# Kernel optimization log

Hardware: AMD Instinct MI355X
Metric: run time of the kernel (lower is better)

Reference implementation:

```python
import jax, jax.numpy as jnp
import numpy as np

NUM_HEADS = 32
HEAD_DIM = 128
HIDDEN = NUM_HEADS * HEAD_DIM  # 4096
ROPE_BASE = 10000.0
VISION_TOKEN_TYPE = 1


def vision_expert_mask(token_type_ids):
    # vision_token_mask[:, :-1] = (tt[:, :-1]==1) & (tt[:, 1:]==1); last col False
    tt = token_type_ids
    m = (tt[:, :-1] == VISION_TOKEN_TYPE) & (tt[:, 1:] == VISION_TOKEN_TYPE)
    return jnp.concatenate([m, jnp.zeros((tt.shape[0], 1), dtype=bool)], axis=1)


def rotary_cos_sin(position_ids, head_dim, dtype):
    inv_freq = 1.0 / (ROPE_BASE ** (jnp.arange(0, head_dim, 2, dtype=jnp.float32) / head_dim))
    freqs = position_ids.astype(jnp.float32)[..., None] * inv_freq  # [B,S,Dh/2]
    emb = jnp.concatenate([freqs, freqs], axis=-1)  # [B,S,Dh]
    return jnp.cos(emb).astype(dtype), jnp.sin(emb).astype(dtype)


def rotate_half(x):
    d = x.shape[-1] // 2
    return jnp.concatenate([-x[..., d:], x[..., :d]], axis=-1)


def setup_inputs() -> dict:
    key = jax.random.key(0)
    ks = jax.random.split(key, 5)
    B, S = 2, 2048
    hidden_states = jax.random.normal(ks[0], (B, S, HIDDEN), dtype=jnp.float32)
    token_type_ids = jax.random.randint(ks[1], (B, S), 0, 2, dtype=jnp.int64)
    position_ids = jnp.broadcast_to(jnp.arange(S, dtype=jnp.int64)[None, :], (B, S))
    scale = 0.02
    w_vis_qkv = jax.random.normal(ks[2], (HIDDEN, 3 * HIDDEN), dtype=jnp.float32) * scale
    w_lang_qkv = jax.random.normal(ks[3], (HIDDEN, 3 * HIDDEN), dtype=jnp.float32) * scale
    w_vis_dense = jax.random.normal(ks[4], (HIDDEN, HIDDEN), dtype=jnp.float32) * scale
    w_lang_dense = jax.random.normal(jax.random.fold_in(key, 7), (HIDDEN, HIDDEN), dtype=jnp.float32) * scale
    return dict(hidden_states=hidden_states, token_type_ids=token_type_ids,
                position_ids=position_ids, w_vis_qkv=w_vis_qkv, w_lang_qkv=w_lang_qkv,
                w_vis_dense=w_vis_dense, w_lang_dense=w_lang_dense)


def reference(hidden_states, token_type_ids, position_ids,
              w_vis_qkv, w_lang_qkv, w_vis_dense, w_lang_dense):
    B, S, D = hidden_states.shape
    vm = vision_expert_mask(token_type_ids)  # [B,S] bool

    # 2-expert QKV dispatch (mask-select between the two expert GEMMs)
    qkv = jnp.where(vm[..., None],
                    hidden_states @ w_vis_qkv,
                    hidden_states @ w_lang_qkv)  # [B,S,3D]
    q, k, v = jnp.split(qkv, 3, axis=-1)
    q = q.reshape(B, S, NUM_HEADS, HEAD_DIM)
    k = k.reshape(B, S, NUM_HEADS, HEAD_DIM)
    v = v.reshape(B, S, NUM_HEADS, HEAD_DIM)

    # rotary embedding on q, k
    cos, sin = rotary_cos_sin(position_ids, HEAD_DIM, q.dtype)  # [B,S,Dh]
    cos, sin = cos[:, :, None, :], sin[:, :, None, :]
    q = q * cos + rotate_half(q) * sin
    k = k * cos + rotate_half(k) * sin

    # causal attention (dense equivalent of the paged-attention call)
    scores = jnp.einsum('bqhd,bkhd->bhqk', q, k) / jnp.sqrt(jnp.array(HEAD_DIM, q.dtype))
    causal = jnp.tril(jnp.ones((S, S), dtype=bool))
    scores = jnp.where(causal[None, None], scores, jnp.finfo(scores.dtype).min)
    probs = jax.nn.softmax(scores, axis=-1)
    ctx = jnp.einsum('bhqk,bkhd->bqhd', probs, v).reshape(B, S, D)

    # 2-expert output dense dispatch
    attn_output = jnp.where(vm[..., None],
                            ctx @ w_vis_dense,
                            ctx @ w_lang_dense)
    return attn_output
```

## Files before the change

### kernel.cpp

```cpp
#include <hip/hip_runtime.h>
#include <math.h>

#define SEQ     2048
#define NB      2
#define NHEADS  32
#define DHEAD   128
#define HID     4096
#define NQKV    12288
#define T_TOKENS (NB*SEQ)

typedef _Float16 half8 __attribute__((ext_vector_type(8)));
typedef float v4f __attribute__((ext_vector_type(4)));

__device__ __forceinline__ void gload_lds16(const void* g, void* l) {
    __builtin_amdgcn_global_load_lds(
        (__attribute__((address_space(1))) void*)(void*)(g),
        (__attribute__((address_space(3))) void*)(unsigned)(unsigned long long)(l),
        16, 0, 0);
}

__device__ __forceinline__ v4f mfma16(half8 a, half8 b, v4f c) {
    return __builtin_amdgcn_mfma_f32_16x16x32_f16(a, b, c, 0, 0, 0);
}

__global__ void route_kernel(const int* __restrict__ tt, int* counts, int* idx) {
    int t = blockIdx.x * blockDim.x + threadIdx.x;
    if (t >= T_TOKENS) return;
    int s = t & (SEQ - 1);
    bool vm = (s < SEQ - 1) && (tt[t] == 1) && (tt[t + 1] == 1);
    int e = vm ? 0 : 1;
    int p = atomicAdd(&counts[e], 1);
    idx[e * T_TOKENS + p] = t;
}

__global__ void rope_table_kernel(const int* __restrict__ pos_ids, float2* __restrict__ tab) {
    int i = blockIdx.x * blockDim.x + threadIdx.x;
    if (i >= T_TOKENS * 64) return;
    int tok = i >> 6, j = i & 63;
    float invf = (float)pow(10000.0, -(double)j * (1.0 / 64.0));
    float ang = (float)pos_ids[tok] * invf;
    double ds, dc;
    sincos((double)ang, &ds, &dc);
    tab[i] = make_float2((float)dc, (float)ds);
}

__global__ void cvt_f32_f16(const float* __restrict__ src, _Float16* __restrict__ dst, int n4) {
    int i = blockIdx.x * blockDim.x + threadIdx.x;
    if (i >= n4) return;
    float4 v = ((const float4*)src)[i];
    union { _Float16 h[4]; uint2 u; } p;
    p.h[0] = (_Float16)v.x; p.h[1] = (_Float16)v.y;
    p.h[2] = (_Float16)v.z; p.h[3] = (_Float16)v.w;
    ((uint2*)dst)[i] = p.u;
}

__global__ void transpose_cvt(const float* __restrict__ W, _Float16* __restrict__ WT,
                              int K, int N) {
    __shared__ _Float16 t[64][72];
    const int n0 = blockIdx.x * 64, k0 = blockIdx.y * 64;
    const int cr = threadIdx.x & 15, rr = threadIdx.x >> 4;
#pragma unroll
    for (int it = 0; it < 4; ++it) {
        int r = rr + it * 16;
        float4 v = *(const float4*)&W[(size_t)(k0 + r) * N + n0 + cr * 4];
        t[cr*4+0][r] = (_Float16)v.x; t[cr*4+1][r] = (_Float16)v.y;
        t[cr*4+2][r] = (_Float16)v.z; t[cr*4+3][r] = (_Float16)v.w;
    }
    __syncthreads();
#pragma unroll
    for (int it = 0; it < 4; ++it) {
        int r = rr + it * 16;
        union { _Float16 h[4]; uint2 u; } p;
#pragma unroll
        for (int j = 0; j < 4; ++j) p.h[j] = t[r][cr*4+j];
        *(uint2*)&WT[(size_t)(n0 + r) * K + k0 + cr * 4] = p.u;
    }
}

__global__ void transpose_v(const _Float16* __restrict__ vin, _Float16* __restrict__ vout) {
    __shared__ _Float16 t[64][72];
    const int s0 = blockIdx.x * 64;
    const int d0 = blockIdx.y * 64;
    const int bh = blockIdx.z;
    const int b = bh >> 5, h = bh & 31;
    const int cr = threadIdx.x & 15, rr = threadIdx.x >> 4;
#pragma unroll
    for (int it = 0; it < 4; ++it) {
        int sl = rr + it * 16;
        union { _Float16 h4[4]; uint2 u; } p;
        p.u = *(const uint2*)&vin[(size_t)(b * SEQ + s0 + sl) * HID + h * DHEAD + d0 + cr * 4];
#pragma unroll
        for (int j = 0; j < 4; ++j) t[cr*4+j][sl] = p.h4[j];
    }
    __syncthreads();
#pragma unroll
    for (int it = 0; it < 4; ++it) {
        int dl = rr + it * 16;
        union { _Float16 h4[4]; uint2 u; } p;
#pragma unroll
        for (int j = 0; j < 4; ++j) p.h4[j] = t[dl][cr*4+j];
        *(uint2*)&vout[((size_t)bh * DHEAD + d0 + dl) * SEQ + s0 + cr * 4] = p.u;
    }
}

template <int MODE, int NCT>
__global__ __launch_bounds__(256, 3)
void gemm_expert(const _Float16* __restrict__ A,
                 const _Float16* __restrict__ BT0,
                 const _Float16* __restrict__ BT1,
                 const int* __restrict__ counts,
                 const int* __restrict__ idx_all,
                 const float2* __restrict__ rope,
                 _Float16* __restrict__ qbuf,
                 _Float16* __restrict__ kbuf,
                 _Float16* __restrict__ vbuf,
                 float* __restrict__ out) {
    const int e = blockIdx.z;
    const int count = counts[e];

    const int f   = blockIdx.x + NCT * blockIdx.y;
    const int xcd = f & 7;
    const int g   = f >> 3;
    const int c   = g >> 6;
    const int wi  = g & 63;
    const int rt  = wi >> 1;
    const int ct  = xcd * (NCT / 8) + c * 2 + (wi & 1);

    if (rt * 128 >= count) return;
    const int* idx = idx_all + e * T_TOKENS;
    const _Float16* BT = e ? BT1 : BT0;

    __shared__ _Float16 sA[3][128 * 32];
    __shared__ _Float16 sB[3][128 * 32];

    const int tid = threadIdx.x;
    const int w = tid >> 6, lane = tid & 63;
    const int col = lane & 15, quad = lane >> 4;
    const int wm = w >> 1, wn = w & 1;

    const int r0 = (w * 2 + 0) * 16 + (lane >> 2);
    const int r1 = (w * 2 + 1) * 16 + (lane >> 2);
    int g0 = rt * 128 + r0; if (g0 > count - 1) g0 = count - 1;
    int g1 = rt * 128 + r1; if (g1 > count - 1) g1 = count - 1;
    const int tok0 = idx[g0], tok1 = idx[g1];
    const int schk = (lane & 3) ^ ((lane >> 3) & 3);
    const _Float16* ag0 = A + (size_t)tok0 * HID + schk * 8;
    const _Float16* ag1 = A + (size_t)tok1 * HID + schk * 8;
    const _Float16* bg0 = BT + (size_t)(ct * 128 + r0) * HID + schk * 8;
    const _Float16* bg1 = BT + (size_t)(ct * 128 + r1) * HID + schk * 8;
    const int sa_off0 = (w * 2 + 0) * 512;
    const int sa_off1 = (w * 2 + 1) * 512;

    v4f acc[4][4];
#pragma unroll
    for (int i = 0; i < 4; ++i)
#pragma unroll
        for (int j = 0; j < 4; ++j) { v4f z = {0.f, 0.f, 0.f, 0.f}; acc[i][j] = z; }

    const int kofq = (quad ^ ((col >> 1) & 3)) * 8;

    auto stage = [&](int buf) {
        gload_lds16(ag0, &sA[buf][sa_off0]); gload_lds16(ag1, &sA[buf][sa_off1]);
        gload_lds16(bg0, &sB[buf][sa_off0]); gload_lds16(bg1, &sB[buf][sa_off1]);
        ag0 += 32; ag1 += 32; bg0 += 32; bg1 += 32;
    };
    auto compute = [&](int cur) {
        half8 a[4], b[4];
#pragma unroll
        for (int i = 0; i < 4; ++i)
            a[i] = *(const half8*)&sA[cur][(wm * 64 + i * 16 + col) * 32 + kofq];
#pragma unroll
        for (int j = 0; j < 4; ++j)
            b[j] = *(const half8*)&sB[cur][((wn + 2 * j) * 16 + col) * 32 + kofq];
#pragma unroll
        for (int i = 0; i < 4; ++i)
#pragma unroll
            for (int j = 0; j < 4; ++j)
                acc[i][j] = mfma16(a[i], b[j], acc[i][j]);
    };

    const int NK = HID / 32;
    stage(0); stage(1);

    int cur = 0, nxt = 2;
    for (int kt = 0; kt < NK - 2; ++kt) {
        asm volatile("s_waitcnt vmcnt(4)" ::: "memory");
        __builtin_amdgcn_s_barrier();
        asm volatile("" ::: "memory");
        stage(nxt);
        compute(cur);
        cur = (cur == 2) ? 0 : cur + 1;
        nxt = (nxt == 2) ? 0 : nxt + 1;
    }
    asm volatile("s_waitcnt vmcnt(4)" ::: "memory");
    __builtin_amdgcn_s_barrier();
    asm volatile("" ::: "memory");
    compute(cur);
    cur = (cur == 2) ? 0 : cur + 1;
    asm volatile("s_waitcnt vmcnt(0)" ::: "memory");
    __builtin_amdgcn_s_barrier();
    asm volatile("" ::: "memory");
    compute(cur);

    const int n0 = ct * 128;
    if (MODE == 1) {
#pragma unroll
        for (int i = 0; i < 4; ++i)
#pragma unroll
            for (int r = 0; r < 4; ++r) {
                int rg = rt * 128 + wm * 64 + i * 16 + quad * 4 + r;
                if (rg >= count) continue;
                int tok = idx[rg];
                float* dst = out + (size_t)tok * HID + n0;
#pragma unroll
                for (int j = 0; j < 4; ++j) dst[(wn + 2 * j) * 16 + col] = acc[i][j][r];
            }
    } else {
        const int sec = n0 >> 12;
        const int h = (n0 >> 7) & 31;
#pragma unroll
        for (int i = 0; i < 4; ++i)
#pragma unroll
            for (int r = 0; r < 4; ++r) {
                int rg = rt * 128 + wm * 64 + i * 16 + quad * 4 + r;
                if (rg >= count) continue;
                int tok = idx[rg];
                int b = tok >> 11, s = tok & (SEQ - 1);
                if (sec == 2) {
                    _Float16* dst = vbuf + (size_t)tok * HID + h * DHEAD;
#pragma unroll
                    for (int j = 0; j < 4; ++j) dst[(wn + 2 * j) * 16 + col] = (_Float16)acc[i][j][r];
                } else {
                    _Float16* dst = (sec ? kbuf : qbuf) + ((size_t)(b * NHEADS + h) * SEQ + s) * DHEAD;
                    const float2* tp = rope + (size_t)tok * 64;
#pragma unroll
                    for (int j = 0; j < 2; ++j) {
                        int d = (wn + 2 * j) * 16 + col;
                        float2 cs = tp[d];
                        float x = acc[i][j][r], y = acc[i][j + 2][r];
                        dst[d]      = (_Float16)(x * cs.x - y * cs.y);
                        dst[d + 64] = (_Float16)(y * cs.x + x * cs.y);
                    }
                }
            }
    }
}

__global__ __launch_bounds__(256, 2)
void attn_kernel(const _Float16* __restrict__ qbuf,
                 const _Float16* __restrict__ kbuf,
                 const _Float16* __restrict__ vt,
                 _Float16* __restrict__ ctx) {
    const int f   = blockIdx.x;
    const int xcd = f & 7;
    const int t   = f >> 3;
    const int s   = t & 31;
    const int rr  = t >> 5;
    const int u   = s & 15, g = s >> 4;
    const int bh  = xcd * 8 + rr * 2 + g;
    const int qt  = (rr & 1) ? (15 - u) : u;

    const int b = bh >> 5, h = bh & 31;
    const int tid = threadIdx.x;
    const int w = tid >> 6, lane = tid & 63;
    const int col = lane & 15, quad = lane >> 4;

    __shared__ _Float16 sK[2][64 * 128];
    __shared__ _Float16 sV[2][128 * 64];
    __shared__ _Float16 sP[128 * 64];

    half8 qf[2][4];
    const _Float16 qscale = (_Float16)0.08838834764831845f;
#pragma unroll
    for (int mt = 0; mt < 2; ++mt)
#pragma unroll
        for (int kc = 0; kc < 4; ++kc) {
            int row = qt * 128 + w * 32 + mt * 16 + col;
            half8 v = *(const half8*)&qbuf[((size_t)bh * SEQ + row) * DHEAD + kc * 32 + quad * 8];
            qf[mt][kc] = v * qscale;
        }

    float mrow[2][4], lrow[2][4];
    v4f o[2][8];
#pragma unroll
    for (int mt = 0; mt < 2; ++mt)
#pragma unroll
        for (int r = 0; r < 4; ++r) { mrow[mt][r] = -3.0e38f; lrow[mt][r] = 0.f; }
#pragma unroll
    for (int i = 0; i < 2; ++i)
#pragma unroll
        for (int j = 0; j < 8; ++j) { v4f z = {0.f, 0.f, 0.f, 0.f}; o[i][j] = z; }

    const int cxor = col & 7;
    const int vs_chk = (lane & 7) ^ (lane >> 3);
    const int nkt = 2 * qt + 2;

    const _Float16* kg0 = kbuf + (size_t)bh * SEQ * DHEAD;
    const _Float16* vg0 = vt + (size_t)bh * DHEAD * SEQ;

    auto stage = [&](int kt, int buf) {
        const _Float16* kg = kg0 + (size_t)kt * 64 * DHEAD;
        const _Float16* vg = vg0 + kt * 64;
#pragma unroll
        for (int op = 0; op < 4; ++op) {
            int r0 = (w * 4 + op) * 4;
            int krow = r0 + quad;
            int kcs = col ^ (krow & 7);
            gload_lds16(kg + (size_t)krow * DHEAD + kcs * 8, &sK[buf][r0 * 128]);
            int d0 = (w * 4 + op) * 8;
            int vrow = d0 + (lane >> 3);
            gload_lds16(vg + (size_t)vrow * SEQ + vs_chk * 8, &sV[buf][d0 * 64]);
        }
    };

    stage(0, 0);
    __syncthreads();

    for (int kt = 0; kt < nkt; ++kt) {
        const int cur = kt & 1;
        if (kt + 1 < nkt) stage(kt + 1, cur ^ 1);

        v4f sc[2][4];
#pragma unroll
        for (int i = 0; i < 2; ++i)
#pragma unroll
            for (int j = 0; j < 4; ++j) { v4f z = {0.f, 0.f, 0.f, 0.f}; sc[i][j] = z; }
#pragma unroll
        for (int kc = 0; kc < 4; ++kc) {
            const int kof = ((kc * 4 + quad) ^ cxor) * 8;
#pragma unroll
            for (int nt = 0; nt < 4; ++nt) {
                half8 bf = *(const half8*)&sK[cur][(size_t)(nt * 16 + col) * 128 + kof];
                sc[0][nt] = mfma16(qf[0][kc], bf, sc[0][nt]);
                sc[1][nt] = mfma16(qf[1][kc], bf, sc[1][nt]);
            }
        }

        if (kt >= 2 * qt) {
#pragma unroll
            for (int mt = 0; mt < 2; ++mt)
#pragma unroll
                for (int nt = 0; nt < 4; ++nt)
#pragma unroll
                    for (int r = 0; r < 4; ++r) {
                        int rowa = qt * 128 + w * 32 + mt * 16 + quad * 4 + r;
                        int cola = kt * 64 + nt * 16 + col;
                        if (cola > rowa) sc[mt][nt][r] = -3.0e38f;
                    }
        }

#pragma unroll
        for (int mt = 0; mt < 2; ++mt)
#pragma unroll
            for (int r = 0; r < 4; ++r) {
                float mx = sc[mt][0][r];
#pragma unroll
                for (int nt = 1; nt < 4; ++nt) mx = fmaxf(mx, sc[mt][nt][r]);
                mx = fmaxf(mx, __shfl_xor(mx, 1));
                mx = fmaxf(mx, __shfl_xor(mx, 2));
                mx = fmaxf(mx, __shfl_xor(mx, 4));
                mx = fmaxf(mx, __shfl_xor(mx, 8));
                float newm = fmaxf(mrow[mt][r], mx);
                float alpha = __expf(mrow[mt][r] - newm);
                mrow[mt][r] = newm;
                float rs = 0.f;
#pragma unroll
                for (int nt = 0; nt < 4; ++nt) {
                    float p = __expf(sc[mt][nt][r] - newm);
                    sc[mt][nt][r] = p;
                    rs += p;
                }
                rs += __shfl_xor(rs, 1); rs += __shfl_xor(rs, 2);
                rs += __shfl_xor(rs, 4); rs += __shfl_xor(rs, 8);
                lrow[mt][r] = lrow[mt][r] * alpha + rs;
#pragma unroll
                for (int nt = 0; nt < 8; ++nt) o[mt][nt][r] *= alpha;
            }

#pragma unroll
        for (int mt = 0; mt < 2; ++mt)
#pragma unroll
            for (int nt = 0; nt < 4; ++nt)
#pragma unroll
                for (int r = 0; r < 4; ++r) {
                    int rp = w * 32 + mt * 16 + quad * 4 + r;
                    int colh = nt * 16 + col;
                    int c = (colh >> 3) ^ (rp & 7);
                    sP[(size_t)rp * 64 + c * 8 + (colh & 7)] = (_Float16)sc[mt][nt][r];
                }

#pragma unroll
        for (int kc = 0; kc < 2; ++kc) {
            const int kof = ((kc * 4 + quad) ^ cxor) * 8;
            half8 p0 = *(const half8*)&sP[(size_t)(w * 32 + col) * 64 + kof];
            half8 p1 = *(const half8*)&sP[(size_t)(w * 32 + 16 + col) * 64 + kof];
#pragma unroll
            for (int nt = 0; nt < 8; ++nt) {
                half8 vf = *(const half8*)&sV[cur][(size_t)(nt * 16 + col) * 64 + kof];
                o[0][nt] = mfma16(p0, vf, o[0][nt]);
                o[1][nt] = mfma16(p1, vf, o[1][nt]);
            }
        }

        __syncthreads();
    }

#pragma unroll
    for (int mt = 0; mt < 2; ++mt)
#pragma unroll
        for (int r = 0; r < 4; ++r) {
            int rowa = qt * 128 + w * 32 + mt * 16 + quad * 4 + r;
            float inv = 1.0f / lrow[mt][r];
            _Float16* dst = ctx + ((size_t)b * SEQ + rowa) * HID + h * DHEAD;
#pragma unroll
            for (int nt = 0; nt < 8; ++nt)
                dst[nt * 16 + col] = (_Float16)(o[mt][nt][r] * inv);
        }
}

extern "C" void kernel_launch(void* const* d_in, const int* in_sizes, int n_in,
                              void* d_out, int out_size, void* d_ws, size_t ws_size,
                              hipStream_t stream) {
    const float* hidden = (const float*)d_in[0];
    const int*   tt     = (const int*)d_in[1];
    const int*   pos    = (const int*)d_in[2];
    const float* wvq    = (const float*)d_in[3];
    const float* wlq    = (const float*)d_in[4];
    const float* wvd    = (const float*)d_in[5];
    const float* wld    = (const float*)d_in[6];
    float* out = (float*)d_out;

    char* ws = (char*)d_ws;
    size_t off = 0;
    auto alloc = [&](size_t bytes) {
        char* p = ws + off;
        off += (bytes + 255) & ~(size_t)255;
        return p;
    };
    const size_t TOKB = (size_t)T_TOKENS * HID * sizeof(_Float16);
    _Float16* h16  = (_Float16*)alloc(TOKB);
    _Float16* wvqT = (_Float16*)alloc((size_t)NQKV * HID * 2);
    _Float16* wlqT = (_Float16*)alloc((size_t)NQKV * HID * 2);
    _Float16* wvdT = (_Float16*)alloc((size_t)HID * HID * 2);
    _Float16* wldT = (_Float16*)alloc((size_t)HID * HID * 2);
    _Float16* qb   = (_Float16*)alloc(TOKB);
    _Float16* kb   = (_Float16*)alloc(TOKB);
    _Float16* vtmp = (_Float16*)alloc(TOKB);
    int* counts = (int*)alloc(2 * sizeof(int));
    int* idx    = (int*)alloc(2 * T_TOKENS * sizeof(int));
    float2* rope = (float2*)alloc((size_t)T_TOKENS * 64 * sizeof(float2));
    _Float16* vT  = h16;
    _Float16* ctx = vtmp;

    hipMemsetAsync(counts, 0, 2 * sizeof(int), stream);
    route_kernel<<<T_TOKENS / 256, 256, 0, stream>>>(tt, counts, idx);
    rope_table_kernel<<<(T_TOKENS * 64) / 256, 256, 0, stream>>>(pos, rope);
    cvt_f32_f16<<<(T_TOKENS * HID / 4) / 256, 256, 0, stream>>>(hidden, h16, T_TOKENS * HID / 4);
    transpose_cvt<<<dim3(NQKV / 64, HID / 64), 256, 0, stream>>>(wvq, wvqT, HID, NQKV);
    transpose_cvt<<<dim3(NQKV / 64, HID / 64), 256, 0, stream>>>(wlq, wlqT, HID, NQKV);
    transpose_cvt<<<dim3(HID / 64, HID / 64), 256, 0, stream>>>(wvd, wvdT, HID, HID);
    transpose_cvt<<<dim3(HID / 64, HID / 64), 256, 0, stream>>>(wld, wldT, HID, HID);
    gemm_expert<0, NQKV / 128><<<dim3(NQKV / 128, T_TOKENS / 128, 2), 256, 0, stream>>>(
        h16, wvqT, wlqT, counts, idx, rope, qb, kb, vtmp, nullptr);
    transpose_v<<<dim3(SEQ / 64, DHEAD / 64, NB * NHEADS), 256, 0, stream>>>(vtmp, vT);
    attn_kernel<<<dim3(16 * NB * NHEADS), 256, 0, stream>>>(qb, kb, vT, ctx);
    gemm_expert<1, HID / 128><<<dim3(HID / 128, T_TOKENS / 128, 2), 256, 0, stream>>>(
        ctx, wvdT, wldT, counts, idx, nullptr, nullptr, nullptr, nullptr, out);
}
```

Before: 1.549 ms.

## Pair causal q-tiles per attention block and raise priority around MFMA

Each attention block now processes two complementary query tiles (u and 15-u) of the same head, sharing each staged K/V tile between them, which balances causal work per block and halves K/V loads. The grid is halved accordingly. s_setprio is raised around the MFMA loops in both the GEMM and attention kernels to favor matrix issue over other waves. Doubling the accumulators and Q fragments raises register pressure and may cause spills or lower occupancy.

Result: slower. 1.913 ms (+23.5%).

```diff
diff --git a/kernel.cpp b/kernel.cpp
--- a/kernel.cpp
+++ b/kernel.cpp
@@ -172,11 +172,13 @@
 #pragma unroll
         for (int j = 0; j < 4; ++j)
             b[j] = *(const half8*)&sB[cur][((wn + 2 * j) * 16 + col) * 32 + kofq];
+        __builtin_amdgcn_s_setprio(1);
 #pragma unroll
         for (int i = 0; i < 4; ++i)
 #pragma unroll
             for (int j = 0; j < 4; ++j)
                 acc[i][j] = mfma16(a[i], b[j], acc[i][j]);
+        __builtin_amdgcn_s_setprio(0);
     };
 
     const int NK = HID / 32;
@@ -254,11 +256,9 @@
     const int f   = blockIdx.x;
     const int xcd = f & 7;
     const int t   = f >> 3;
-    const int s   = t & 31;
-    const int rr  = t >> 5;
-    const int u   = s & 15, g = s >> 4;
-    const int bh  = xcd * 8 + rr * 2 + g;
-    const int qt  = (rr & 1) ? (15 - u) : u;
+    const int u   = t & 7;
+    const int bh  = xcd * 8 + (t >> 3);
+    const int qtA = u, qtB = 15 - u;
 
     const int b = bh >> 5, h = bh & 31;
     const int tid = threadIdx.x;
@@ -269,31 +269,39 @@
     __shared__ _Float16 sV[2][128 * 64];
     __shared__ _Float16 sP[128 * 64];
 
-    half8 qf[2][4];
     const _Float16 qscale = (_Float16)0.08838834764831845f;
+    half8 qfA[2][4], qfB[2][4];
 #pragma unroll
     for (int mt = 0; mt < 2; ++mt)
 #pragma unroll
         for (int kc = 0; kc < 4; ++kc) {
-            int row = qt * 128 + w * 32 + mt * 16 + col;
-            half8 v = *(const half8*)&qbuf[((size_t)bh * SEQ + row) * DHEAD + kc * 32 + quad * 8];
-            qf[mt][kc] = v * qscale;
-        }
-
-    float mrow[2][4], lrow[2][4];
-    v4f o[2][8];
+            int rowA = qtA * 128 + w * 32 + mt * 16 + col;
+            qfA[mt][kc] = *(const half8*)&qbuf[((size_t)bh * SEQ + rowA) * DHEAD + kc * 32 + quad * 8] * qscale;
+            int rowB = qtB * 128 + w * 32 + mt * 16 + col;
+            qfB[mt][kc] = *(const half8*)&qbuf[((size_t)bh * SEQ + rowB) * DHEAD + kc * 32 + quad * 8] * qscale;
+        }
+
+    float mA[2][4], lA[2][4], mB[2][4], lB[2][4];
+    v4f oA[2][8], oB[2][8];
 #pragma unroll
     for (int mt = 0; mt < 2; ++mt)
 #pragma unroll
-        for (int r = 0; r < 4; ++r) { mrow[mt][r] = -3.0e38f; lrow[mt][r] = 0.f; }
+        for (int r = 0; r < 4; ++r) {
+            mA[mt][r] = -3.0e38f; lA[mt][r] = 0.f;
+            mB[mt][r] = -3.0e38f; lB[mt][r] = 0.f;
+        }
 #pragma unroll
     for (int i = 0; i < 2; ++i)
 #pragma unroll
-        for (int j = 0; j < 8; ++j) { v4f z = {0.f, 0.f, 0.f, 0.f}; o[i][j] = z; }
+        for (int j = 0; j < 8; ++j) {
+            v4f z = {0.f, 0.f, 0.f, 0.f};
+            oA[i][j] = z; oB[i][j] = z;
+        }
 
     const int cxor = col & 7;
     const int vs_chk = (lane & 7) ^ (lane >> 3);
-    const int nkt = 2 * qt + 2;
+    const int nkt  = 2 * qtB + 2;
+    const int nktA = 2 * qtA + 2;
 
     const _Float16* kg0 = kbuf + (size_t)bh * SEQ * DHEAD;
     const _Float16* vg0 = vt + (size_t)bh * DHEAD * SEQ;
@@ -313,18 +321,14 @@
         }
     };
 
-    stage(0, 0);
-    __syncthreads();
-
-    for (int kt = 0; kt < nkt; ++kt) {
-        const int cur = kt & 1;
-        if (kt + 1 < nkt) stage(kt + 1, cur ^ 1);
-
+    auto proc = [&](const half8 (&qf)[2][4], float (&mrow)[2][4], float (&lrow)[2][4],
+                    v4f (&o)[2][8], int qt, int kt, int cur) {
         v4f sc[2][4];
 #pragma unroll
         for (int i = 0; i < 2; ++i)
 #pragma unroll
             for (int j = 0; j < 4; ++j) { v4f z = {0.f, 0.f, 0.f, 0.f}; sc[i][j] = z; }
+        __builtin_amdgcn_s_setprio(1);
 #pragma unroll
         for (int kc = 0; kc < 4; ++kc) {
             const int kof = ((kc * 4 + quad) ^ cxor) * 8;
@@ -335,6 +339,7 @@
                 sc[1][nt] = mfma16(qf[1][kc], bf, sc[1][nt]);
             }
         }
+        __builtin_amdgcn_s_setprio(0);
 
         if (kt >= 2 * qt) {
 #pragma unroll
@@ -389,6 +394,7 @@
                     sP[(size_t)rp * 64 + c * 8 + (colh & 7)] = (_Float16)sc[mt][nt][r];
                 }
 
+        __builtin_amdgcn_s_setprio(1);
 #pragma unroll
         for (int kc = 0; kc < 2; ++kc) {
             const int kof = ((kc * 4 + quad) ^ cxor) * 8;
@@ -401,21 +407,35 @@
                 o[1][nt] = mfma16(p1, vf, o[1][nt]);
             }
         }
-
+        __builtin_amdgcn_s_setprio(0);
+    };
+
+    stage(0, 0);
+    __syncthreads();
+
+    for (int kt = 0; kt < nkt; ++kt) {
+        const int cur = kt & 1;
+        if (kt + 1 < nkt) stage(kt + 1, cur ^ 1);
+        proc(qfB, mB, lB, oB, qtB, kt, cur);
+        if (kt < nktA) proc(qfA, mA, lA, oA, qtA, kt, cur);
         __syncthreads();
     }
 
-#pragma unroll
-    for (int mt = 0; mt < 2; ++mt)
-#pragma unroll
-        for (int r = 0; r < 4; ++r) {
-            int rowa = qt * 128 + w * 32 + mt * 16 + quad * 4 + r;
-            float inv = 1.0f / lrow[mt][r];
-            _Float16* dst = ctx + ((size_t)b * SEQ + rowa) * HID + h * DHEAD;
-#pragma unroll
-            for (int nt = 0; nt < 8; ++nt)
-                dst[nt * 16 + col] = (_Float16)(o[mt][nt][r] * inv);
-        }
+    auto writeo = [&](float (&lrow)[2][4], v4f (&o)[2][8], int qt) {
+#pragma unroll
+        for (int mt = 0; mt < 2; ++mt)
+#pragma unroll
+            for (int r = 0; r < 4; ++r) {
+                int rowa = qt * 128 + w * 32 + mt * 16 + quad * 4 + r;
+                float inv = 1.0f / lrow[mt][r];
+                _Float16* dst = ctx + ((size_t)b * SEQ + rowa) * HID + h * DHEAD;
+#pragma unroll
+                for (int nt = 0; nt < 8; ++nt)
+                    dst[nt * 16 + col] = (_Float16)(o[mt][nt][r] * inv);
+            }
+    };
+    writeo(lA, oA, qtA);
+    writeo(lB, oB, qtB);
 }
 
 extern "C" void kernel_launch(void* const* d_in, const int* in_sizes, int n_in,
@@ -463,7 +483,7 @@
     gemm_expert<0, NQKV / 128><<<dim3(NQKV / 128, T_TOKENS / 128, 2), 256, 0, stream>>>(
         h16, wvqT, wlqT, counts, idx, rope, qb, kb, vtmp, nullptr);
     transpose_v<<<dim3(SEQ / 64, DHEAD / 64, NB * NHEADS), 256, 0, stream>>>(vtmp, vT);
-    attn_kernel<<<dim3(16 * NB * NHEADS), 256, 0, stream>>>(qb, kb, vT, ctx);
+    attn_kernel<<<dim3(8 * NB * NHEADS), 256, 0, stream>>>(qb, kb, vT, ctx);
     gemm_expert<1, HID / 128><<<dim3(HID / 128, T_TOKENS / 128, 2), 256, 0, stream>>>(
         ctx, wvdT, wldT, counts, idx, nullptr, nullptr, nullptr, nullptr, out);
 }
```
